# Performance work log

Hardware: AMD Instinct MI355X
Metric: run time of the kernel (lower is better)

Reference implementation:

```python
import jax, jax.numpy as jnp
import numpy as np

HIDDEN = 256

def setup_inputs() -> dict:
    key = jax.random.key(0)
    k1, k2, k3, k4 = jax.random.split(key, 4)
    B, S, H = 64, 4096, HIDDEN
    o_all_time = jax.random.normal(k1, (B, S, H), dtype=jnp.float32)
    scale = 1.0 / np.sqrt(H)
    W_t = jax.random.uniform(k2, (H, H), dtype=jnp.float32, minval=-scale, maxval=scale)
    W_F = jax.random.uniform(k3, (H, H), dtype=jnp.float32, minval=-scale, maxval=scale)
    v_F = jax.random.uniform(k4, (H, 1), dtype=jnp.float32, minval=-scale, maxval=scale)
    return {"o_all_time": o_all_time, "W_t": W_t, "W_F": W_F, "v_F": v_F}

def reference(o_all_time, W_t, W_F, v_F):
    # o_all_time: (B, S, H)
    o_last = o_all_time[:, -1, :]                       # (B, H)
    # time attention: scores = o_last @ (o_all_time @ W_t)^T over seq
    M_t = jnp.einsum('bsh,hk->bsk', o_all_time, W_t)    # (B, S, H)
    scores_time = jnp.einsum('bh,bsh->bs', o_last, M_t) # (B, S)
    alpha_t = jax.nn.softmax(scores_time, axis=-1)      # (B, S)
    output_T = jnp.einsum('bs,bsh->bh', alpha_t, o_all_time)  # (B, H)
    # feature attention: softmax over seq of v_F^T tanh(W_F x)
    M_f = jnp.tanh(jnp.einsum('bsh,hk->bsk', o_all_time, W_F))  # (B, S, H)
    scores_feature = jnp.einsum('bsh,hk->bsk', M_f, v_F)[..., 0]  # (B, S)
    alpha_f = jax.nn.softmax(scores_feature, axis=1)    # (B, S)
    output_F = jnp.einsum('bs,bsh->bh', alpha_f, o_all_time)  # (B, H)
    return jnp.concatenate([output_T, output_F], axis=1)  # (B, 2H)
```

## Files before the change

### kernel.cpp

```cpp
#include <hip/hip_runtime.h>
#include <hip/hip_bf16.h>
#include <stdint.h>

#define HID 256
#define BATCH 64
#define SEQ 4096

typedef __attribute__((ext_vector_type(8))) short bf16x8;
typedef __attribute__((ext_vector_type(4))) short short4v;
typedef __attribute__((ext_vector_type(4))) float f32x4;

static __device__ __forceinline__ unsigned short f2bf(float f) {
    union { float f; uint32_t u; } v; v.f = f;
    uint32_t u = v.u;
    return (unsigned short)((u + 0x7FFF + ((u >> 16) & 1)) >> 16);
}

static __device__ __forceinline__ float fast_tanh(float x) {
    float cx = fminf(fmaxf(x, -15.f), 15.f);
    float e = __expf(2.f * cx);
    return (e - 1.f) / (e + 1.f);
}

__global__ __launch_bounds__(256) void prep_wft(const float* __restrict__ WF,
                                                unsigned short* __restrict__ WFt) {
    int c = blockIdx.x, h = threadIdx.x;
    WFt[c * HID + h] = f2bf(WF[h * HID + c]);
}

__global__ __launch_bounds__(256) void prep_ut(const float* __restrict__ o,
                                               const float* __restrict__ Wt,
                                               float* __restrict__ ut) {
    __shared__ float ol[HID];
    int b = blockIdx.x, h = threadIdx.x;
    ol[h] = o[(size_t)(b * SEQ + SEQ - 1) * HID + h];
    __syncthreads();
    const float* wrow = Wt + h * HID;
    float acc = 0.f;
    #pragma unroll 8
    for (int k = 0; k < HID; k++) acc += wrow[k] * ol[k];
    ut[b * HID + h] = acc;
}

__global__ __launch_bounds__(256) void scores_kernel(const float* __restrict__ o,
                                                     const unsigned short* __restrict__ WFt,
                                                     const float* __restrict__ ut,
                                                     const float* __restrict__ vF,
                                                     float* __restrict__ stOut,
                                                     float* __restrict__ sfOut) {
    __shared__ unsigned short o_sm[64 * HID];
    __shared__ float u_sm[HID];
    __shared__ float stp[64 * 64];
    __shared__ float red[4 * 64];
    __shared__ float sfr[4 * 64];

    int t = threadIdx.x;
    int lane = t & 63, w = t >> 6;
    int bid = blockIdx.x;
    int b = bid >> 6;
    int s0 = (bid & 63) << 6;

    u_sm[t] = ut[b * HID + t];
    __syncthreads();

    const float* obase = o + (size_t)(b * SEQ + s0) * HID;
    const float4 u4 = *(const float4*)&u_sm[lane << 2];

    #pragma unroll 4
    for (int j = 0; j < 16; j++) {
        int e = j * 1024 + t * 4;
        float4 v = *(const float4*)(obase + e);
        int row = j * 4 + w;
        float d = v.x * u4.x + v.y * u4.y + v.z * u4.z + v.w * u4.w;
        stp[(row << 6) + (lane ^ (row & 31))] = d;
        int byte = (row << 9) + (lane << 3);
        byte ^= (row & 7) << 4;
        short4v sv;
        sv.x = (short)f2bf(v.x); sv.y = (short)f2bf(v.y);
        sv.z = (short)f2bf(v.z); sv.w = (short)f2bf(v.w);
        *(short4v*)((char*)o_sm + byte) = sv;
    }
    __syncthreads();

    {
        int r = lane, part = w;
        float ssum = 0.f;
        #pragma unroll
        for (int i = 0; i < 16; i++) {
            int c = part * 16 + i;
            ssum += stp[(r << 6) + (c ^ (r & 31))];
        }
        red[part * 64 + r] = ssum;
    }

    f32x4 acc[4][4];
    #pragma unroll
    for (int ar = 0; ar < 4; ar++)
        #pragma unroll
        for (int cb = 0; cb < 4; cb++)
            acc[ar][cb] = (f32x4){0.f, 0.f, 0.f, 0.f};

    int cw = w << 6;
    int lm = lane & 15, lg = lane >> 4;

    #pragma unroll
    for (int kk = 0; kk < 8; kk++) {
        int h0 = kk * 32 + lg * 8;
        bf16x8 bf[4], af[4];
        #pragma unroll
        for (int cb = 0; cb < 4; cb++) {
            int c = cw + cb * 16 + lm;
            bf[cb] = *(const bf16x8*)(WFt + (size_t)c * HID + h0);
        }
        #pragma unroll
        for (int ar = 0; ar < 4; ar++) {
            int row = ar * 16 + lm;
            int byte = (row << 9) + h0 * 2;
            byte ^= (row & 7) << 4;
            af[ar] = *(const bf16x8*)((const char*)o_sm + byte);
        }
        #pragma unroll
        for (int ar = 0; ar < 4; ar++)
            #pragma unroll
            for (int cb = 0; cb < 4; cb++)
                acc[ar][cb] = __builtin_amdgcn_mfma_f32_16x16x32_bf16(af[ar], bf[cb], acc[ar][cb], 0, 0, 0);
    }

    __syncthreads();
    if (t < 64) {
        float s = red[t] + red[64 + t] + red[128 + t] + red[192 + t];
        stOut[(size_t)b * SEQ + s0 + t] = s;
    }

    float vf[4];
    #pragma unroll
    for (int cb = 0; cb < 4; cb++) vf[cb] = vF[cw + cb * 16 + lm];

    #pragma unroll
    for (int ar = 0; ar < 4; ar++) {
        #pragma unroll
        for (int i = 0; i < 4; i++) {
            float p = 0.f;
            #pragma unroll
            for (int cb = 0; cb < 4; cb++)
                p += fast_tanh(acc[ar][cb][i]) * vf[cb];
            p += __shfl_xor(p, 1);
            p += __shfl_xor(p, 2);
            p += __shfl_xor(p, 4);
            p += __shfl_xor(p, 8);
            if (lm == 0) sfr[w * 64 + ar * 16 + lg * 4 + i] = p;
        }
    }
    __syncthreads();
    if (t < 64) {
        float s = sfr[t] + sfr[64 + t] + sfr[128 + t] + sfr[192 + t];
        sfOut[(size_t)b * SEQ + s0 + t] = s;
    }
}

template <bool MAXOP>
static __device__ __forceinline__ float block_reduce(float v, float* sh) {
    #pragma unroll
    for (int m = 1; m < 64; m <<= 1) {
        float o = __shfl_xor(v, m);
        v = MAXOP ? fmaxf(v, o) : (v + o);
    }
    int w = threadIdx.x >> 6;
    if ((threadIdx.x & 63) == 0) sh[w] = v;
    __syncthreads();
    float r = MAXOP ? fmaxf(fmaxf(sh[0], sh[1]), fmaxf(sh[2], sh[3]))
                    : (sh[0] + sh[1] + sh[2] + sh[3]);
    __syncthreads();
    return r;
}

__global__ __launch_bounds__(256) void stats_kernel(const float* __restrict__ st,
                                                    const float* __restrict__ sf,
                                                    float* __restrict__ stats) {
    __shared__ float sh[4];
    int b = blockIdx.x, t = threadIdx.x;
    const float* pt = st + (size_t)b * SEQ;
    const float* pf = sf + (size_t)b * SEQ;
    float vt[16], vf[16], mT = -1e30f, mF = -1e30f;
    #pragma unroll
    for (int j = 0; j < 16; j++) {
        vt[j] = pt[t + j * 256]; mT = fmaxf(mT, vt[j]);
        vf[j] = pf[t + j * 256]; mF = fmaxf(mF, vf[j]);
    }
    mT = block_reduce<true>(mT, sh);
    mF = block_reduce<true>(mF, sh);
    float sT = 0.f, sF = 0.f;
    #pragma unroll
    for (int j = 0; j < 16; j++) {
        sT += __expf(vt[j] - mT);
        sF += __expf(vf[j] - mF);
    }
    sT = block_reduce<false>(sT, sh);
    sF = block_reduce<false>(sF, sh);
    if (t == 0) {
        stats[b * 4 + 0] = mT;
        stats[b * 4 + 1] = sT;
        stats[b * 4 + 2] = mF;
        stats[b * 4 + 3] = sF;
    }
}

__global__ __launch_bounds__(256) void out_kernel(const float* __restrict__ o,
                                                  const float* __restrict__ st,
                                                  const float* __restrict__ sf,
                                                  const float* __restrict__ stats,
                                                  float* __restrict__ out) {
    __shared__ float wT[256], wF[256];
    __shared__ float4 redT[4][64], redF[4][64];
    int bid = blockIdx.x;
    int b = bid >> 4, chunk = bid & 15, s0 = chunk << 8;
    int t = threadIdx.x;

    float mT = stats[b * 4 + 0], isT = 1.f / stats[b * 4 + 1];
    float mF = stats[b * 4 + 2], isF = 1.f / stats[b * 4 + 3];
    wT[t] = __expf(st[(size_t)b * SEQ + s0 + t] - mT) * isT;
    wF[t] = __expf(sf[(size_t)b * SEQ + s0 + t] - mF) * isF;
    __syncthreads();

    int hc = t & 63, sl = t >> 6;
    const float* ob = o + (size_t)(b * SEQ + s0) * HID + hc * 4;
    float4 aT = {0.f, 0.f, 0.f, 0.f}, aF = {0.f, 0.f, 0.f, 0.f};
    #pragma unroll 4
    for (int s = sl; s < 256; s += 4) {
        float4 v = *(const float4*)(ob + (size_t)s * HID);
        float wt = wT[s], wf = wF[s];
        aT.x += wt * v.x; aT.y += wt * v.y; aT.z += wt * v.z; aT.w += wt * v.w;
        aF.x += wf * v.x; aF.y += wf * v.y; aF.z += wf * v.z; aF.w += wf * v.w;
    }
    redT[sl][hc] = aT;
    redF[sl][hc] = aF;
    __syncthreads();

    int hcc = t >> 2, i = t & 3;
    float sumT = 0.f, sumF = 0.f;
    #pragma unroll
    for (int p = 0; p < 4; p++) {
        sumT += ((const float*)&redT[p][hcc])[i];
        sumF += ((const float*)&redF[p][hcc])[i];
    }
    atomicAdd(out + (size_t)b * 512 + t, sumT);
    atomicAdd(out + (size_t)b * 512 + 256 + t, sumF);
}

extern "C" void kernel_launch(void* const* d_in, const int* in_sizes, int n_in,
                              void* d_out, int out_size, void* d_ws, size_t ws_size,
                              hipStream_t stream) {
    const float* o  = (const float*)d_in[0];
    const float* Wt = (const float*)d_in[1];
    const float* WF = (const float*)d_in[2];
    const float* vF = (const float*)d_in[3];
    float* out = (float*)d_out;
    char* ws = (char*)d_ws;

    unsigned short* WFt = (unsigned short*)ws;
    float* ut    = (float*)(ws + 131072);
    float* stS   = (float*)(ws + 196608);
    float* sfS   = (float*)(ws + 196608 + 1048576);
    float* stats = (float*)(ws + 196608 + 2097152);

    hipMemsetAsync(d_out, 0, (size_t)BATCH * 512 * sizeof(float), stream);
    prep_wft<<<256, 256, 0, stream>>>(WF, WFt);
    prep_ut<<<BATCH, 256, 0, stream>>>(o, Wt, ut);
    scores_kernel<<<BATCH * 64, 256, 0, stream>>>(o, WFt, ut, vF, stS, sfS);
    stats_kernel<<<BATCH, 256, 0, stream>>>(stS, sfS, stats);
    out_kernel<<<BATCH * 16, 256, 0, stream>>>(o, stS, sfS, stats, out);
}
```

Baseline: 483.0 us.

## Batch global loads, shuffle-reduce time scores, and split out_kernel finer

In scores_kernel, all 16 float4 rows are loaded up front into registers so more memory requests are in flight at once. The time-score dot products are now reduced with wave shuffles instead of a 64x64 shared scratch tile and second pass, which frees LDS and drops a barrier. out_kernel switches to 128-row chunks, doubling its grid, and batches 8 loads per iteration. Both kernels get launch_bounds occupancy hints, at the cost of higher register pressure and twice as many atomic adds.

```diff
diff --git a/kernel.cpp b/kernel.cpp
--- a/kernel.cpp
+++ b/kernel.cpp
@@ -42,16 +42,15 @@
     ut[b * HID + h] = acc;
 }
 
-__global__ __launch_bounds__(256) void scores_kernel(const float* __restrict__ o,
-                                                     const unsigned short* __restrict__ WFt,
-                                                     const float* __restrict__ ut,
-                                                     const float* __restrict__ vF,
-                                                     float* __restrict__ stOut,
-                                                     float* __restrict__ sfOut) {
+__global__ __launch_bounds__(256, 4) void scores_kernel(const float* __restrict__ o,
+                                                        const unsigned short* __restrict__ WFt,
+                                                        const float* __restrict__ ut,
+                                                        const float* __restrict__ vF,
+                                                        float* __restrict__ stOut,
+                                                        float* __restrict__ sfOut) {
     __shared__ unsigned short o_sm[64 * HID];
     __shared__ float u_sm[HID];
-    __shared__ float stp[64 * 64];
-    __shared__ float red[4 * 64];
+    __shared__ float red_sm[64 * 4];
     __shared__ float sfr[4 * 64];
 
     int t = threadIdx.x;
@@ -59,20 +58,30 @@
     int bid = blockIdx.x;
     int b = bid >> 6;
     int s0 = (bid & 63) << 6;
+    int lm = lane & 15, lg = lane >> 4;
 
     u_sm[t] = ut[b * HID + t];
     __syncthreads();
 
-    const float* obase = o + (size_t)(b * SEQ + s0) * HID;
+    const float* pbase = o + (size_t)(b * SEQ + s0) * HID + t * 4;
     const float4 u4 = *(const float4*)&u_sm[lane << 2];
 
-    #pragma unroll 4
+    float4 va[8], vb[8];
+    #pragma unroll
+    for (int j = 0; j < 8; j++) va[j] = *(const float4*)(pbase + j * 1024);
+    #pragma unroll
+    for (int j = 0; j < 8; j++) vb[j] = *(const float4*)(pbase + (j + 8) * 1024);
+
+    #pragma unroll
     for (int j = 0; j < 16; j++) {
-        int e = j * 1024 + t * 4;
-        float4 v = *(const float4*)(obase + e);
+        float4 v = (j < 8) ? va[j & 7] : vb[j & 7];
         int row = j * 4 + w;
-        float d = v.x * u4.x + v.y * u4.y + v.z * u4.z + v.w * u4.w;
-        stp[(row << 6) + (lane ^ (row & 31))] = d;
+        float p = v.x * u4.x + v.y * u4.y + v.z * u4.z + v.w * u4.w;
+        p += __shfl_xor(p, 1);
+        p += __shfl_xor(p, 2);
+        p += __shfl_xor(p, 4);
+        p += __shfl_xor(p, 8);
+        if (lm == 0) red_sm[(row << 2) + lg] = p;
         int byte = (row << 9) + (lane << 3);
         byte ^= (row & 7) << 4;
         short4v sv;
@@ -82,15 +91,9 @@
     }
     __syncthreads();
 
-    {
-        int r = lane, part = w;
-        float ssum = 0.f;
-        #pragma unroll
-        for (int i = 0; i < 16; i++) {
-            int c = part * 16 + i;
-            ssum += stp[(r << 6) + (c ^ (r & 31))];
-        }
-        red[part * 64 + r] = ssum;
+    if (t < 64) {
+        const float* r4 = &red_sm[t << 2];
+        stOut[(size_t)b * SEQ + s0 + t] = r4[0] + r4[1] + r4[2] + r4[3];
     }
 
     f32x4 acc[4][4];
@@ -101,7 +104,6 @@
             acc[ar][cb] = (f32x4){0.f, 0.f, 0.f, 0.f};
 
     int cw = w << 6;
-    int lm = lane & 15, lg = lane >> 4;
 
     #pragma unroll
     for (int kk = 0; kk < 8; kk++) {
@@ -124,12 +126,6 @@
             #pragma unroll
             for (int cb = 0; cb < 4; cb++)
                 acc[ar][cb] = __builtin_amdgcn_mfma_f32_16x16x32_bf16(af[ar], bf[cb], acc[ar][cb], 0, 0, 0);
-    }
-
-    __syncthreads();
-    if (t < 64) {
-        float s = red[t] + red[64 + t] + red[128 + t] + red[192 + t];
-        stOut[(size_t)b * SEQ + s0 + t] = s;
     }
 
     float vf[4];
@@ -205,32 +201,43 @@
     }
 }
 
-__global__ __launch_bounds__(256) void out_kernel(const float* __restrict__ o,
-                                                  const float* __restrict__ st,
-                                                  const float* __restrict__ sf,
-                                                  const float* __restrict__ stats,
-                                                  float* __restrict__ out) {
-    __shared__ float wT[256], wF[256];
+__global__ __launch_bounds__(256, 4) void out_kernel(const float* __restrict__ o,
+                                                     const float* __restrict__ st,
+                                                     const float* __restrict__ sf,
+                                                     const float* __restrict__ stats,
+                                                     float* __restrict__ out) {
+    __shared__ float wT[128], wF[128];
     __shared__ float4 redT[4][64], redF[4][64];
     int bid = blockIdx.x;
-    int b = bid >> 4, chunk = bid & 15, s0 = chunk << 8;
+    int b = bid >> 5, chunk = bid & 31, s0 = chunk << 7;
     int t = threadIdx.x;
 
-    float mT = stats[b * 4 + 0], isT = 1.f / stats[b * 4 + 1];
-    float mF = stats[b * 4 + 2], isF = 1.f / stats[b * 4 + 3];
-    wT[t] = __expf(st[(size_t)b * SEQ + s0 + t] - mT) * isT;
-    wF[t] = __expf(sf[(size_t)b * SEQ + s0 + t] - mF) * isF;
+    if (t < 128) {
+        float mT = stats[b * 4 + 0], isT = 1.f / stats[b * 4 + 1];
+        float mF = stats[b * 4 + 2], isF = 1.f / stats[b * 4 + 3];
+        wT[t] = __expf(st[(size_t)b * SEQ + s0 + t] - mT) * isT;
+        wF[t] = __expf(sf[(size_t)b * SEQ + s0 + t] - mF) * isF;
+    }
     __syncthreads();
 
     int hc = t & 63, sl = t >> 6;
     const float* ob = o + (size_t)(b * SEQ + s0) * HID + hc * 4;
     float4 aT = {0.f, 0.f, 0.f, 0.f}, aF = {0.f, 0.f, 0.f, 0.f};
-    #pragma unroll 4
-    for (int s = sl; s < 256; s += 4) {
-        float4 v = *(const float4*)(ob + (size_t)s * HID);
-        float wt = wT[s], wf = wF[s];
-        aT.x += wt * v.x; aT.y += wt * v.y; aT.z += wt * v.z; aT.w += wt * v.w;
-        aF.x += wf * v.x; aF.y += wf * v.y; aF.z += wf * v.z; aF.w += wf * v.w;
+    #pragma unroll
+    for (int ii = 0; ii < 4; ii++) {
+        float4 v[8];
+        #pragma unroll
+        for (int k = 0; k < 8; k++) {
+            int r = sl + (ii * 8 + k) * 4;
+            v[k] = *(const float4*)(ob + (size_t)r * HID);
+        }
+        #pragma unroll
+        for (int k = 0; k < 8; k++) {
+            int r = sl + (ii * 8 + k) * 4;
+            float wt = wT[r], wf = wF[r];
+            aT.x += wt * v[k].x; aT.y += wt * v[k].y; aT.z += wt * v[k].z; aT.w += wt * v[k].w;
+            aF.x += wf * v[k].x; aF.y += wf * v[k].y; aF.z += wf * v[k].z; aF.w += wf * v[k].w;
+        }
     }
     redT[sl][hc] = aT;
     redF[sl][hc] = aF;
@@ -268,5 +275,5 @@
     prep_ut<<<BATCH, 256, 0, stream>>>(o, Wt, ut);
     scores_kernel<<<BATCH * 64, 256, 0, stream>>>(o, WFt, ut, vF, stS, sfS);
     stats_kernel<<<BATCH, 256, 0, stream>>>(stS, sfS, stats);
-    out_kernel<<<BATCH * 16, 256, 0, stream>>>(o, stS, sfS, stats, out);
-}
+    out_kernel<<<BATCH * 32, 256, 0, stream>>>(o, stS, sfS, stats, out);
+}
```

After: 460.8 us. -4.6%, faster.
